# Performance work log

Hardware: AMD Instinct MI355X
Metric: run time of the kernel (lower is better)

Reference implementation:

```python
import jax, jax.numpy as jnp
import numpy as np
from jax import lax

EPS = 1e-07
B, H, W = 32, 120, 120
N_PRIM, PRIM_DIM = 16, 8          # 16 capsule types, 8-d pose
N_SEC, SEC_DIM = 10, 16           # 10 secondary capsules, 16-d
FLAT = 9216                       # 16 * 24 * 24
R_ITERS = 3
REC_DIM = H * W * 3               # 43200


def _conv(x, w, b, stride):
    # NHWC input, HWIO kernel, VALID padding
    y = lax.conv_general_dilated(x, w, (stride, stride), 'VALID',
                                 dimension_numbers=('NHWC', 'HWIO', 'NHWC'))
    return y + b


def _squash(s):
    s_norm = jnp.linalg.norm(s, axis=-1, keepdims=True)
    sq = jnp.square(s_norm)
    return sq / (1.0 + sq) * s / (s_norm + EPS)


def setup_inputs() -> dict:
    key = jax.random.key(0)
    ks = jax.random.split(key, 13)
    p = lambda k, shp, s=0.05: (jax.random.normal(k, shp, dtype=jnp.float32) * s)
    inp = {
        'input_x': jax.random.normal(ks[0], (B, H, W, 3), dtype=jnp.float32),
        'y':       jax.random.uniform(ks[1], (B, N_SEC), dtype=jnp.float32),
        'conv1_w': p(ks[2], (9, 9, 3, 256)),
        'conv1_b': jnp.zeros((256,), jnp.float32),
        'conv2_w': p(ks[3], (9, 9, 256, N_PRIM * PRIM_DIM)),
        'conv2_b': jnp.zeros((N_PRIM * PRIM_DIM,), jnp.float32),
        'w_pose':  p(ks[4], (1, FLAT, N_SEC, SEC_DIM, PRIM_DIM)),
        'w1': p(ks[5], (N_SEC * SEC_DIM, 512)), 'b1': jnp.zeros((512,), jnp.float32),
        'w2': p(ks[6], (512, 1024)),            'b2': jnp.zeros((1024,), jnp.float32),
        'w3': p(ks[7], (1024, REC_DIM)),        'b3': jnp.zeros((REC_DIM,), jnp.float32),
    }
    return inp


def reference(input_x, y, conv1_w, conv1_b, conv2_w, conv2_b, w_pose,
              w1, b1, w2, b2, w3, b3):
    b = input_x.shape[0]
    # feature extraction
    x = jax.nn.relu(_conv(input_x, conv1_w, conv1_b, 2))   # [B,56,56,256]
    x = _conv(x, conv2_w, conv2_b, 2)                      # [B,24,24,128]
    u = x.reshape(b, FLAT, PRIM_DIM)                       # [B,9216,8]
    # u_hat[b,n,c,d] = sum_p w_pose[0,n,c,d,p] * u[b,n,p]
    u_hat = jnp.einsum('ncdp,bnp->bncd', w_pose[0], u)     # [B,9216,10,16]
    # dynamic routing
    logits = jnp.zeros((b, FLAT, N_SEC, 1), jnp.float32)
    v = None
    for _ in range(R_ITERS):
        c = jax.nn.softmax(logits, axis=-2)                # over secondary caps
        s = jnp.sum(c * u_hat, axis=1, keepdims=True)      # [B,1,10,16]
        v = _squash(s)
        agreement = jnp.sum(u_hat * v, axis=-1, keepdims=True)  # [B,9216,10,1]
        logits = logits + agreement
    # masking + reconstruction
    mask = y[:, None, :, None]                             # [B,1,10,1]
    v_flat = (mask * v).reshape(b, -1)                     # [B,160]
    h = jax.nn.relu(v_flat @ w1 + b1)
    h = jax.nn.relu(h @ w2 + b2)
    rec = jax.nn.sigmoid(h @ w3 + b3)                      # [B,43200]
    return v, rec
```

## Files before the change

### kernel.cpp

```cpp
#include <hip/hip_runtime.h>
#include <hip/hip_bf16.h>

typedef unsigned short u16;
typedef unsigned int   u32;
typedef __attribute__((ext_vector_type(8))) __bf16 bf16x8;
typedef __attribute__((ext_vector_type(4))) float  f32x4;

#define EPSQ 1e-7f
#define KSPLIT 6
#define KPB 3456
#define KSTEPS 108

#define GLDS16(gp, lp) __builtin_amdgcn_global_load_lds( \
    (const __attribute__((address_space(1))) void*)(gp), \
    (__attribute__((address_space(3))) void*)(lp), 16, 0, 0)

__device__ __forceinline__ u16 f2bf(float f){
  u32 u = __float_as_uint(f);
  u32 r = (u + 0x7fffu + ((u >> 16) & 1u)) >> 16;
  return (u16)r;
}
__device__ __forceinline__ float bf2f(u16 h){ return __uint_as_float(((u32)h) << 16); }
__device__ __forceinline__ float blo(u32 w){ return __uint_as_float(w << 16); }
__device__ __forceinline__ float bhi(u32 w){ return __uint_as_float(w & 0xffff0000u); }

__global__ __launch_bounds__(256) void k_im2col(const float* __restrict__ x, u16* __restrict__ A1){
  const int id = blockIdx.x*256 + threadIdx.x;
  const int m  = id >> 5;
  const int s  = id & 31;
  const int b  = m / 3136;
  const int r  = m - b*3136;
  const int oy = r / 56;
  const int ox = r - oy*56;
  const float* xb = x + ((size_t)b*120 + 2*oy)*120*3 + 2*ox*3;
  u16 vals[8];
  #pragma unroll
  for (int j=0;j<8;++j){
    int k = s*8 + j;
    if (k < 243){
      int ky = k / 27;
      int rem = k - ky*27;
      vals[j] = f2bf(xb[(size_t)ky*360 + rem]);
    } else vals[j] = 0;
  }
  *reinterpret_cast<uint4*>(A1 + (size_t)m*256 + s*8) = *reinterpret_cast<uint4*>(vals);
}

__global__ __launch_bounds__(256) void k_wt1(const float* __restrict__ w, u16* __restrict__ wt){
  __shared__ float tile[32][33];
  const int k0 = blockIdx.x*32;
  const int c0 = blockIdx.y*32;
  const int c  = threadIdx.x & 31;
  const int r8 = threadIdx.x >> 5;
  #pragma unroll
  for (int rr=0; rr<4; ++rr){
    int r = r8*4+rr;
    tile[r][c] = (k0+r < 243) ? w[(size_t)(k0+r)*256 + c0 + c] : 0.f;
  }
  __syncthreads();
  #pragma unroll
  for (int rr=0; rr<4; ++rr){
    int r = r8*4+rr;
    wt[(size_t)(c0+r)*256 + k0 + c] = f2bf(tile[c][r]);
  }
}

__global__ __launch_bounds__(256) void k_gemm1(const u16* __restrict__ A1,
    const u16* __restrict__ w1t, const float* __restrict__ bias, u16* __restrict__ a1b){
  __shared__ __align__(16) u16 As[2][4096];
  __shared__ __align__(16) u16 Bs[2][4096];
  const int t  = threadIdx.x;
  const int bx = blockIdx.x;
  const int by = blockIdx.y;
  const int row0 = t>>2, slot = t&3;
  const int wid = t>>6, lane = t&63;
  const int wr = wid>>1, wc = wid&1, lr = lane&15, lq = lane>>4;
  const size_t srcA0 = (size_t)(bx*128 + row0)*256 + slot*8;
  const size_t srcA1 = srcA0 + (size_t)64*256;
  const size_t srcB0 = (size_t)(by*128 + row0)*256 + slot*8;
  const size_t srcB1 = srcB0 + (size_t)64*256;
  f32x4 acc[4][4];
  #pragma unroll
  for (int i=0;i<4;++i)
    #pragma unroll
    for (int j=0;j<4;++j) acc[i][j] = (f32x4){0.f,0.f,0.f,0.f};

  auto stage = [&](int step, int buf){
    const int k0 = step*32;
    GLDS16(A1 + srcA0 + k0, &As[buf][wid*512]);
    GLDS16(A1 + srcA1 + k0, &As[buf][wid*512 + 2048]);
    GLDS16(w1t + srcB0 + k0, &Bs[buf][wid*512]);
    GLDS16(w1t + srcB1 + k0, &Bs[buf][wid*512 + 2048]);
  };
  auto compute = [&](int buf){
    bf16x8 af[4], bfv[4];
    #pragma unroll
    for (int mi=0;mi<4;++mi)
      af[mi] = *reinterpret_cast<const bf16x8*>(&As[buf][(wr*64 + mi*16 + lr)*32 + lq*8]);
    #pragma unroll
    for (int ni=0;ni<4;++ni)
      bfv[ni] = *reinterpret_cast<const bf16x8*>(&Bs[buf][(wc*64 + ni*16 + lr)*32 + lq*8]);
    #pragma unroll
    for (int mi=0;mi<4;++mi)
      #pragma unroll
      for (int ni=0;ni<4;++ni)
        acc[mi][ni] = __builtin_amdgcn_mfma_f32_16x16x32_bf16(af[mi], bfv[ni], acc[mi][ni], 0, 0, 0);
  };

  stage(0, 0);
  __syncthreads();
  for (int step=0; step<8; step+=2){
    stage(step+1, 1);
    compute(0);
    __syncthreads();
    if (step+2 < 8) stage(step+2, 0);
    compute(1);
    __syncthreads();
  }

  #pragma unroll
  for (int ni=0;ni<4;++ni){
    int colg = by*128 + wc*64 + ni*16 + lr;
    float bv = bias[colg];
    #pragma unroll
    for (int mi=0;mi<4;++mi){
      #pragma unroll
      for (int r=0;r<4;++r){
        int rowg = bx*128 + wr*64 + mi*16 + lq*4 + r;
        float v = fmaxf(acc[mi][ni][r] + bv, 0.f);
        a1b[(size_t)rowg*256 + colg] = f2bf(v);
      }
    }
  }
}

__global__ __launch_bounds__(256) void k_wt(const float* __restrict__ w, u16* __restrict__ wt){
  __shared__ float tile[32][33];
  const int k0 = blockIdx.x*32;
  const int c0 = blockIdx.y*32;
  const int c  = threadIdx.x & 31;
  const int r8 = threadIdx.x >> 5;
  #pragma unroll
  for (int rr=0; rr<4; ++rr){
    int r = r8*4+rr;
    tile[r][c] = w[(size_t)(k0+r)*128 + c0 + c];
  }
  __syncthreads();
  #pragma unroll
  for (int rr=0; rr<4; ++rr){
    int r = r8*4+rr;
    wt[(size_t)(c0+r)*20736 + k0 + c] = f2bf(tile[c][r]);
  }
}

__global__ __launch_bounds__(256) void k_conv2(const u16* __restrict__ a1b,
    const u16* __restrict__ w2t, float* __restrict__ part){
  __shared__ __align__(16) u16 As[2][4096];
  __shared__ __align__(16) u16 Bs[2][4096];
  const int t  = threadIdx.x;
  const int bx = blockIdx.x;
  const int ks = blockIdx.y;
  const int row0 = t>>2, slot = t&3;
  int gA[2]; int gB[2];
  #pragma unroll
  for (int q=0;q<2;++q){
    int m  = bx*128 + row0 + q*64;
    int bb = m/576; int r = m - bb*576; int oy = r/24; int ox = r - oy*24;
    gA[q] = ((bb*56 + 2*oy)*56 + 2*ox)*256 + slot*8;
    int col = row0 + q*64;
    gB[q] = col*20736 + slot*8;
  }
  const int wid = t>>6, lane = t&63;
  const int wr = wid>>1, wc = wid&1, lr = lane&15, lq = lane>>4;
  f32x4 acc[4][4];
  #pragma unroll
  for (int i=0;i<4;++i)
    #pragma unroll
    for (int j=0;j<4;++j) acc[i][j] = (f32x4){0.f,0.f,0.f,0.f};
  const int kbase = ks*KPB;

  auto stage = [&](int step, int buf){
    const int k0  = kbase + step*32;
    const int kk  = k0 >> 8;
    const int ky  = kk/9;
    const int kx  = kk - ky*9;
    const int ic0 = k0 & 255;
    const int soff = (ky*56 + kx)*256 + ic0;
    GLDS16(a1b + gA[0] + soff, &As[buf][wid*512]);
    GLDS16(a1b + gA[1] + soff, &As[buf][wid*512 + 2048]);
    GLDS16(w2t + gB[0] + k0,  &Bs[buf][wid*512]);
    GLDS16(w2t + gB[1] + k0,  &Bs[buf][wid*512 + 2048]);
  };
  auto compute = [&](int buf){
    bf16x8 af[4], bfv[4];
    #pragma unroll
    for (int mi=0;mi<4;++mi)
      af[mi] = *reinterpret_cast<const bf16x8*>(&As[buf][(wr*64 + mi*16 + lr)*32 + lq*8]);
    #pragma unroll
    for (int ni=0;ni<4;++ni)
      bfv[ni] = *reinterpret_cast<const bf16x8*>(&Bs[buf][(wc*64 + ni*16 + lr)*32 + lq*8]);
    #pragma unroll
    for (int mi=0;mi<4;++mi)
      #pragma unroll
      for (int ni=0;ni<4;++ni)
        acc[mi][ni] = __builtin_amdgcn_mfma_f32_16x16x32_bf16(af[mi], bfv[ni], acc[mi][ni], 0, 0, 0);
  };

  stage(0, 0);
  __syncthreads();
  for (int step=0; step<KSTEPS; step+=2){
    stage(step+1, 1);
    compute(0);
    __syncthreads();
    if (step+2 < KSTEPS) stage(step+2, 0);
    compute(1);
    __syncthreads();
  }

  const size_t base = ((size_t)ks*18432 + (size_t)bx*128)*128;
  #pragma unroll
  for (int mi=0;mi<4;++mi){
    #pragma unroll
    for (int ni=0;ni<4;++ni){
      int col = wc*64 + ni*16 + lr;
      #pragma unroll
      for (int r=0;r<4;++r){
        int row = wr*64 + mi*16 + lq*4 + r;
        part[base + (size_t)row*128 + col] = acc[mi][ni][r];
      }
    }
  }
}

__global__ __launch_bounds__(256) void k_comb(const float* __restrict__ part,
    const float* __restrict__ bias, float* __restrict__ u){
  int i = blockIdx.x*256 + threadIdx.x;
  int oc = i & 127;
  float s = bias[oc];
  #pragma unroll
  for (int ks=0; ks<KSPLIT; ++ks) s += part[(size_t)ks*2359296 + i];
  u[i] = s;
}

__global__ __launch_bounds__(256) void k_uhat(const float* __restrict__ u,
    const float* __restrict__ wpose, u16* __restrict__ uhat){
  __shared__ float Wn[1280];
  __shared__ float us[256];
  const int n = blockIdx.x;
  const int t = threadIdx.x;
  #pragma unroll
  for (int j=0;j<5;++j) Wn[t + j*256] = wpose[(size_t)n*1280 + t + j*256];
  us[t] = u[((size_t)(t>>3)*9216 + n)*8 + (t&7)];
  __syncthreads();
  const int b = t>>3, d0 = (t&7)*2;
  float uv[8];
  #pragma unroll
  for (int p=0;p<8;++p) uv[p] = us[b*8+p];
  for (int c=0;c<10;++c){
    const float* w0 = &Wn[(c*16 + d0)*8];
    float v0=0.f, v1=0.f;
    #pragma unroll
    for (int p=0;p<8;++p){ v0 = fmaf(w0[p], uv[p], v0); v1 = fmaf(w0[8+p], uv[p], v1); }
    u32 pk = (u32)f2bf(v0) | ((u32)f2bf(v1) << 16);
    *reinterpret_cast<u32*>(uhat + ((((size_t)b*10 + c)*9216 + n)*16 + d0)) = pk;
  }
}

template<int ITER>
__global__ __launch_bounds__(256) void k_route(const u16* __restrict__ uhat,
    const float* __restrict__ vprev, float* __restrict__ logi,
    float* __restrict__ spart){
  const int ch = blockIdx.x;
  const int b  = blockIdx.y;
  const int t  = threadIdx.x;
  const int n  = ch*256 + t;
  __shared__ float vl[160];
  __shared__ float wlds[10][257];
  if (ITER >= 2){
    if (t < 160) vl[t] = vprev[(size_t)b*160 + t];
  }
  __syncthreads();
  float w[10];
  if (ITER == 1){
    #pragma unroll
    for (int c=0;c<10;++c) w[c] = 0.1f;
  } else {
    float l[10];
    #pragma unroll
    for (int c=0;c<10;++c){
      const u16* up = uhat + ((((size_t)b*10 + c)*9216 + n) << 4);
      const uint4 q0 = *reinterpret_cast<const uint4*>(up);
      const uint4 q1 = *reinterpret_cast<const uint4*>(up + 8);
      const float* v = &vl[c*16];
      float dot = blo(q0.x)*v[0] + bhi(q0.x)*v[1]
                + blo(q0.y)*v[2] + bhi(q0.y)*v[3]
                + blo(q0.z)*v[4] + bhi(q0.z)*v[5]
                + blo(q0.w)*v[6] + bhi(q0.w)*v[7]
                + blo(q1.x)*v[8] + bhi(q1.x)*v[9]
                + blo(q1.y)*v[10]+ bhi(q1.y)*v[11]
                + blo(q1.z)*v[12]+ bhi(q1.z)*v[13]
                + blo(q1.w)*v[14]+ bhi(q1.w)*v[15];
      size_t li = ((size_t)b*10 + c)*9216 + n;
      float lc = dot;
      if (ITER == 3) lc += logi[li];
      if (ITER == 2) logi[li] = lc;
      l[c] = lc;
    }
    float mx = l[0];
    #pragma unroll
    for (int c=1;c<10;++c) mx = fmaxf(mx, l[c]);
    float s = 0.f;
    #pragma unroll
    for (int c=0;c<10;++c){ w[c] = __expf(l[c]-mx); s += w[c]; }
    float inv = 1.f/s;
    #pragma unroll
    for (int c=0;c<10;++c) w[c] *= inv;
  }
  #pragma unroll
  for (int c=0;c<10;++c) wlds[c][t] = w[c];
  __syncthreads();
  if (t < 160){
    const int c = t >> 4, d = t & 15;
    const u16* up = uhat + ((((size_t)b*10 + c)*9216 + (size_t)ch*256) << 4) + d;
    float acc = 0.f;
    #pragma unroll 8
    for (int j=0;j<256;++j)
      acc = fmaf(wlds[c][j], bf2f(up[(size_t)j << 4]), acc);
    spart[((size_t)ch*32 + b)*160 + t] = acc;
  }
}

__global__ __launch_bounds__(256) void k_squash(const float* __restrict__ spart,
    float* __restrict__ vbuf, float* __restrict__ dout_v, int final_){
  const int b = blockIdx.x;
  const int t = threadIdx.x;
  __shared__ float sq[160];
  float sv = 0.f;
  if (t < 160){
    #pragma unroll 4
    for (int ch=0; ch<36; ++ch) sv += spart[((size_t)ch*32 + b)*160 + t];
    sq[t] = sv*sv;
  }
  __syncthreads();
  if (t < 160){
    int cc = t >> 4;
    float ss = 0.f;
    #pragma unroll
    for (int j=0;j<16;++j) ss += sq[cc*16 + j];
    float nrm = sqrtf(ss);
    float vv = (ss/(1.f+ss)) * sv / (nrm + EPSQ);
    vbuf[(size_t)b*160 + t] = vv;
    if (final_) dout_v[(size_t)b*160 + t] = vv;
  }
}

__global__ __launch_bounds__(512) void k_fc1(const float* __restrict__ y,
    const float* __restrict__ vbuf, const float* __restrict__ w1,
    const float* __restrict__ b1, float* __restrict__ h1){
  const int b = blockIdx.x, t = threadIdx.x;
  __shared__ float vf[160];
  if (t < 160) vf[t] = y[b*10 + (t>>4)] * vbuf[(size_t)b*160 + t];
  __syncthreads();
  float acc = b1[t];
  for (int k=0;k<160;++k) acc = fmaf(vf[k], w1[(size_t)k*512 + t], acc);
  h1[(size_t)b*512 + t] = fmaxf(acc, 0.f);
}

__global__ __launch_bounds__(1024) void k_fc2(const float* __restrict__ h1,
    const float* __restrict__ w2, const float* __restrict__ b2, float* __restrict__ h2){
  const int b = blockIdx.x, t = threadIdx.x;
  __shared__ float hs[512];
  if (t < 512) hs[t] = h1[(size_t)b*512 + t];
  __syncthreads();
  float acc = b2[t];
  for (int k=0;k<512;++k) acc = fmaf(hs[k], w2[(size_t)k*1024 + t], acc);
  h2[(size_t)b*1024 + t] = fmaxf(acc, 0.f);
}

__global__ __launch_bounds__(256) void k_fc3p(const float* __restrict__ h2,
    const float* __restrict__ w3, float* __restrict__ fp){
  __shared__ float hs[256][33];
  const int t  = threadIdx.x;
  const int oc = blockIdx.x*256 + t;
  const int ks = blockIdx.y;
  #pragma unroll
  for (int j=0;j<32;++j) hs[t][j] = h2[(size_t)j*1024 + ks*256 + t];
  __syncthreads();
  const bool ok = oc < 43200;
  float a[32];
  #pragma unroll
  for (int b=0;b<32;++b) a[b] = 0.f;
  const size_t wbase = (size_t)ks*256*43200 + (size_t)(ok ? oc : 0);
  #pragma unroll 4
  for (int k=0;k<256;++k){
    float wv = w3[wbase + (size_t)k*43200];
    #pragma unroll
    for (int b=0;b<32;++b) a[b] = fmaf(hs[k][b], wv, a[b]);
  }
  if (ok){
    #pragma unroll
    for (int b=0;b<32;++b) fp[(size_t)(ks*32 + b)*43200 + oc] = a[b];
  }
}

__global__ __launch_bounds__(256) void k_fc3f(const float* __restrict__ fp,
    const float* __restrict__ b3, float* __restrict__ outr){
  int i = blockIdx.x*256 + threadIdx.x;
  if (i >= 32*43200) return;
  int b = i/43200, oc = i - b*43200;
  float s = b3[oc];
  #pragma unroll
  for (int ks=0;ks<4;++ks) s += fp[(size_t)(ks*32 + b)*43200 + oc];
  outr[i] = 1.f/(1.f + __expf(-s));
}

extern "C" void kernel_launch(void* const* d_in, const int* in_sizes, int n_in,
                              void* d_out, int out_size, void* d_ws, size_t ws_size,
                              hipStream_t stream){
  (void)in_sizes; (void)n_in; (void)out_size; (void)ws_size;
  const float* x     = (const float*)d_in[0];
  const float* y     = (const float*)d_in[1];
  const float* c1w   = (const float*)d_in[2];
  const float* c1b   = (const float*)d_in[3];
  const float* c2w   = (const float*)d_in[4];
  const float* c2b   = (const float*)d_in[5];
  const float* wpose = (const float*)d_in[6];
  const float* w1    = (const float*)d_in[7];
  const float* b1    = (const float*)d_in[8];
  const float* w2    = (const float*)d_in[9];
  const float* b2    = (const float*)d_in[10];
  const float* w3    = (const float*)d_in[11];
  const float* b3    = (const float*)d_in[12];
  float* out = (float*)d_out;

  char* ws = (char*)d_ws;
  u16*   A1col = (u16*)(ws + 0);
  float* partp = (float*)(ws + 0);
  u16*   a1bp  = (u16*)(ws + 57000000);
  u16*   uhatp = (u16*)(ws + 0);
  u16*   w1tp  = (u16*)(ws + 109000000);
  u16*   w2tp  = (u16*)(ws + 109200000);
  float* up    = (float*)(ws + 114600000);
  float* logip = (float*)(ws + 124100000);
  float* spartp= (float*)(ws + 136000000);
  float* vbufp = (float*)(ws + 137000000);
  float* h1p   = (float*)(ws + 137100000);
  float* h2p   = (float*)(ws + 137200000);
  float* fc3pp = (float*)(ws + 137400000);

  k_im2col<<<dim3(12544),  256, 0, stream>>>(x, A1col);
  k_wt1   <<<dim3(8,8),    256, 0, stream>>>(c1w, w1tp);
  k_wt    <<<dim3(648,4),  256, 0, stream>>>(c2w, w2tp);
  k_gemm1 <<<dim3(784,2),  256, 0, stream>>>(A1col, w1tp, c1b, a1bp);
  k_conv2 <<<dim3(144,KSPLIT), 256, 0, stream>>>(a1bp, w2tp, partp);
  k_comb  <<<dim3(9216),   256, 0, stream>>>(partp, c2b, up);
  k_uhat  <<<dim3(9216),   256, 0, stream>>>(up, wpose, uhatp);

  k_route<1><<<dim3(36,32), 256, 0, stream>>>(uhatp, vbufp, logip, spartp);
  k_squash  <<<dim3(32),    256, 0, stream>>>(spartp, vbufp, out, 0);
  k_route<2><<<dim3(36,32), 256, 0, stream>>>(uhatp, vbufp, logip, spartp);
  k_squash  <<<dim3(32),    256, 0, stream>>>(spartp, vbufp, out, 0);
  k_route<3><<<dim3(36,32), 256, 0, stream>>>(uhatp, vbufp, logip, spartp);
  k_squash  <<<dim3(32),    256, 0, stream>>>(spartp, vbufp, out, 1);

  k_fc1 <<<dim3(32),    512,  0, stream>>>(y, vbufp, w1, b1, h1p);
  k_fc2 <<<dim3(32),    1024, 0, stream>>>(h1p, w2, b2, h2p);
  k_fc3p<<<dim3(169,4), 256,  0, stream>>>(h2p, w3, fc3pp);
  k_fc3f<<<dim3(5400),  256,  0, stream>>>(fc3pp, b3, out + 5120);
}
```

Baseline: 581.4 us.

## Fuse squash into routing and head, split conv2 and fc3 further

The squash step now runs inside the next routing kernel, and the final squash plus fc1 and fc2 are merged into one head kernel. This removes five small launches and their round trips through global memory. The conv2 K-split goes from 6 to 9 and the fc3 K-split from 4 to 8 to put more blocks in flight, and h2 is stored transposed so fc3 can stage it with float4 loads. The cost is more partial sums to combine, redundant squash work in every routing block, and a reshuffled workspace layout.

Measured after the change: 542.5 us. -6.7%, faster.

```diff
diff --git a/kernel.cpp b/kernel.cpp
--- a/kernel.cpp
+++ b/kernel.cpp
@@ -7,9 +7,10 @@
 typedef __attribute__((ext_vector_type(4))) float  f32x4;
 
 #define EPSQ 1e-7f
-#define KSPLIT 6
-#define KPB 3456
-#define KSTEPS 108
+#define KSPLIT 9
+#define KPB 2304
+#define KSTEPS 72
+#define FC3SPL 8
 
 #define GLDS16(gp, lp) __builtin_amdgcn_global_load_lds( \
     (const __attribute__((address_space(1))) void*)(gp), \
@@ -268,18 +269,33 @@
 
 template<int ITER>
 __global__ __launch_bounds__(256) void k_route(const u16* __restrict__ uhat,
-    const float* __restrict__ vprev, float* __restrict__ logi,
-    float* __restrict__ spart){
+    const float* __restrict__ spin, float* __restrict__ logi,
+    float* __restrict__ spout){
   const int ch = blockIdx.x;
   const int b  = blockIdx.y;
   const int t  = threadIdx.x;
   const int n  = ch*256 + t;
   __shared__ float vl[160];
+  __shared__ float sq[160];
   __shared__ float wlds[10][257];
   if (ITER >= 2){
-    if (t < 160) vl[t] = vprev[(size_t)b*160 + t];
-  }
-  __syncthreads();
+    float sv = 0.f;
+    if (t < 160){
+      #pragma unroll 4
+      for (int c2=0;c2<36;++c2) sv += spin[((size_t)c2*32 + b)*160 + t];
+      sq[t] = sv*sv;
+    }
+    __syncthreads();
+    if (t < 160){
+      int cc = t >> 4;
+      float ss = 0.f;
+      #pragma unroll
+      for (int j=0;j<16;++j) ss += sq[cc*16 + j];
+      float nrm = sqrtf(ss);
+      vl[t] = (ss/(1.f+ss)) * sv / (nrm + EPSQ);
+    }
+    __syncthreads();
+  }
   float w[10];
   if (ITER == 1){
     #pragma unroll
@@ -326,19 +342,24 @@
     #pragma unroll 8
     for (int j=0;j<256;++j)
       acc = fmaf(wlds[c][j], bf2f(up[(size_t)j << 4]), acc);
-    spart[((size_t)ch*32 + b)*160 + t] = acc;
-  }
-}
-
-__global__ __launch_bounds__(256) void k_squash(const float* __restrict__ spart,
-    float* __restrict__ vbuf, float* __restrict__ dout_v, int final_){
+    spout[((size_t)ch*32 + b)*160 + t] = acc;
+  }
+}
+
+__global__ __launch_bounds__(1024) void k_head(const float* __restrict__ y,
+    const float* __restrict__ spin, const float* __restrict__ w1,
+    const float* __restrict__ b1, const float* __restrict__ w2,
+    const float* __restrict__ b2, float* __restrict__ dout_v,
+    float* __restrict__ h2T){
   const int b = blockIdx.x;
   const int t = threadIdx.x;
+  __shared__ float vl[160];
   __shared__ float sq[160];
+  __shared__ float h1s[512];
   float sv = 0.f;
   if (t < 160){
     #pragma unroll 4
-    for (int ch=0; ch<36; ++ch) sv += spart[((size_t)ch*32 + b)*160 + t];
+    for (int c2=0;c2<36;++c2) sv += spin[((size_t)c2*32 + b)*160 + t];
     sq[t] = sv*sv;
   }
   __syncthreads();
@@ -349,53 +370,48 @@
     for (int j=0;j<16;++j) ss += sq[cc*16 + j];
     float nrm = sqrtf(ss);
     float vv = (ss/(1.f+ss)) * sv / (nrm + EPSQ);
-    vbuf[(size_t)b*160 + t] = vv;
-    if (final_) dout_v[(size_t)b*160 + t] = vv;
-  }
-}
-
-__global__ __launch_bounds__(512) void k_fc1(const float* __restrict__ y,
-    const float* __restrict__ vbuf, const float* __restrict__ w1,
-    const float* __restrict__ b1, float* __restrict__ h1){
-  const int b = blockIdx.x, t = threadIdx.x;
-  __shared__ float vf[160];
-  if (t < 160) vf[t] = y[b*10 + (t>>4)] * vbuf[(size_t)b*160 + t];
-  __syncthreads();
-  float acc = b1[t];
-  for (int k=0;k<160;++k) acc = fmaf(vf[k], w1[(size_t)k*512 + t], acc);
-  h1[(size_t)b*512 + t] = fmaxf(acc, 0.f);
-}
-
-__global__ __launch_bounds__(1024) void k_fc2(const float* __restrict__ h1,
-    const float* __restrict__ w2, const float* __restrict__ b2, float* __restrict__ h2){
-  const int b = blockIdx.x, t = threadIdx.x;
-  __shared__ float hs[512];
-  if (t < 512) hs[t] = h1[(size_t)b*512 + t];
+    dout_v[(size_t)b*160 + t] = vv;
+    vl[t] = vv * y[b*10 + cc];
+  }
+  __syncthreads();
+  if (t < 512){
+    float acc = b1[t];
+    for (int k=0;k<160;++k) acc = fmaf(vl[k], w1[(size_t)k*512 + t], acc);
+    h1s[t] = fmaxf(acc, 0.f);
+  }
   __syncthreads();
   float acc = b2[t];
-  for (int k=0;k<512;++k) acc = fmaf(hs[k], w2[(size_t)k*1024 + t], acc);
-  h2[(size_t)b*1024 + t] = fmaxf(acc, 0.f);
-}
-
-__global__ __launch_bounds__(256) void k_fc3p(const float* __restrict__ h2,
+  for (int k=0;k<512;++k) acc = fmaf(h1s[k], w2[(size_t)k*1024 + t], acc);
+  h2T[(size_t)t*32 + b] = fmaxf(acc, 0.f);
+}
+
+__global__ __launch_bounds__(256) void k_fc3p(const float* __restrict__ h2T,
     const float* __restrict__ w3, float* __restrict__ fp){
-  __shared__ float hs[256][33];
+  __shared__ float4 hs4[128][8];
   const int t  = threadIdx.x;
   const int oc = blockIdx.x*256 + t;
   const int ks = blockIdx.y;
-  #pragma unroll
-  for (int j=0;j<32;++j) hs[t][j] = h2[(size_t)j*1024 + ks*256 + t];
+  const float4* src = reinterpret_cast<const float4*>(h2T + (size_t)ks*128*32);
+  #pragma unroll
+  for (int r=0;r<4;++r)
+    (&hs4[0][0])[t + r*256] = src[t + r*256];
   __syncthreads();
   const bool ok = oc < 43200;
   float a[32];
   #pragma unroll
   for (int b=0;b<32;++b) a[b] = 0.f;
-  const size_t wbase = (size_t)ks*256*43200 + (size_t)(ok ? oc : 0);
+  const size_t wbase = (size_t)ks*128*43200 + (size_t)(ok ? oc : 0);
   #pragma unroll 4
-  for (int k=0;k<256;++k){
+  for (int k=0;k<128;++k){
     float wv = w3[wbase + (size_t)k*43200];
     #pragma unroll
-    for (int b=0;b<32;++b) a[b] = fmaf(hs[k][b], wv, a[b]);
+    for (int q=0;q<8;++q){
+      float4 hv = hs4[k][q];
+      a[q*4+0] = fmaf(hv.x, wv, a[q*4+0]);
+      a[q*4+1] = fmaf(hv.y, wv, a[q*4+1]);
+      a[q*4+2] = fmaf(hv.z, wv, a[q*4+2]);
+      a[q*4+3] = fmaf(hv.w, wv, a[q*4+3]);
+    }
   }
   if (ok){
     #pragma unroll
@@ -410,7 +426,7 @@
   int b = i/43200, oc = i - b*43200;
   float s = b3[oc];
   #pragma unroll
-  for (int ks=0;ks<4;++ks) s += fp[(size_t)(ks*32 + b)*43200 + oc];
+  for (int ks=0;ks<FC3SPL;++ks) s += fp[(size_t)(ks*32 + b)*43200 + oc];
   outr[i] = 1.f/(1.f + __expf(-s));
 }
 
@@ -434,19 +450,18 @@
   float* out = (float*)d_out;
 
   char* ws = (char*)d_ws;
-  u16*   A1col = (u16*)(ws + 0);
-  float* partp = (float*)(ws + 0);
-  u16*   a1bp  = (u16*)(ws + 57000000);
+  u16*   a1bp  = (u16*)(ws + 0);
+  u16*   A1col = (u16*)(ws + 52000000);
+  float* partp = (float*)(ws + 52000000);
   u16*   uhatp = (u16*)(ws + 0);
-  u16*   w1tp  = (u16*)(ws + 109000000);
-  u16*   w2tp  = (u16*)(ws + 109200000);
-  float* up    = (float*)(ws + 114600000);
-  float* logip = (float*)(ws + 124100000);
-  float* spartp= (float*)(ws + 136000000);
-  float* vbufp = (float*)(ws + 137000000);
-  float* h1p   = (float*)(ws + 137100000);
-  float* h2p   = (float*)(ws + 137200000);
-  float* fc3pp = (float*)(ws + 137400000);
+  u16*   w1tp  = (u16*)(ws + 138000000);
+  u16*   w2tp  = (u16*)(ws + 138500000);
+  float* up    = (float*)(ws + 144000000);
+  float* logip = (float*)(ws + 154000000);
+  float* spA   = (float*)(ws + 166000000);
+  float* spB   = (float*)(ws + 166800000);
+  float* h2Tp  = (float*)(ws + 167600000);
+  float* fc3pp = (float*)(ws + 0);
 
   k_im2col<<<dim3(12544),  256, 0, stream>>>(x, A1col);
   k_wt1   <<<dim3(8,8),    256, 0, stream>>>(c1w, w1tp);
@@ -456,15 +471,11 @@
   k_comb  <<<dim3(9216),   256, 0, stream>>>(partp, c2b, up);
   k_uhat  <<<dim3(9216),   256, 0, stream>>>(up, wpose, uhatp);
 
-  k_route<1><<<dim3(36,32), 256, 0, stream>>>(uhatp, vbufp, logip, spartp);
-  k_squash  <<<dim3(32),    256, 0, stream>>>(spartp, vbufp, out, 0);
-  k_route<2><<<dim3(36,32), 256, 0, stream>>>(uhatp, vbufp, logip, spartp);
-  k_squash  <<<dim3(32),    256, 0, stream>>>(spartp, vbufp, out, 0);
-  k_route<3><<<dim3(36,32), 256, 0, stream>>>(uhatp, vbufp, logip, spartp);
-  k_squash  <<<dim3(32),    256, 0, stream>>>(spartp, vbufp, out, 1);
-
-  k_fc1 <<<dim3(32),    512,  0, stream>>>(y, vbufp, w1, b1, h1p);
-  k_fc2 <<<dim3(32),    1024, 0, stream>>>(h1p, w2, b2, h2p);
-  k_fc3p<<<dim3(169,4), 256,  0, stream>>>(h2p, w3, fc3pp);
-  k_fc3f<<<dim3(5400),  256,  0, stream>>>(fc3pp, b3, out + 5120);
-}
+  k_route<1><<<dim3(36,32), 256, 0, stream>>>(uhatp, spB, logip, spA);
+  k_route<2><<<dim3(36,32), 256, 0, stream>>>(uhatp, spA, logip, spB);
+  k_route<3><<<dim3(36,32), 256, 0, stream>>>(uhatp, spB, logip, spA);
+
+  k_head <<<dim3(32),   1024, 0, stream>>>(y, spA, w1, b1, w2, b2, out, h2Tp);
+  k_fc3p <<<dim3(169,FC3SPL), 256, 0, stream>>>(h2Tp, w3, fc3pp);
+  k_fc3f <<<dim3(5400), 256, 0, stream>>>(fc3pp, b3, out + 5120);
+}
```
